# Optimization experiments

Hardware: AMD Instinct MI355X
Metric: run time of the kernel (lower is better)

## Reference

```python
import jax, jax.numpy as jnp
import numpy as np

EMBED_DIM = 1024
NUM_HEADS = 16
N = 32768


def setup_inputs() -> dict:
    key = jax.random.key(0)
    k1, k2, k3 = jax.random.split(key, 3)
    h = jax.random.normal(k1, (N, EMBED_DIM), dtype=jnp.float32)
    # torch nn.Linear(E, 3E): weight [3E, E], bias [3E] (bias=True by default)
    W_qkv = jax.random.normal(k2, (3 * EMBED_DIM, EMBED_DIM), dtype=jnp.float32) * 0.02
    b_qkv = jax.random.normal(k3, (3 * EMBED_DIM,), dtype=jnp.float32) * 0.02
    return {"h": h, "W_qkv": W_qkv, "b_qkv": b_qkv}


def reference(h, W_qkv, b_qkv):
    n, e = h.shape
    head_dim = e // NUM_HEADS
    # fused QKV projection: [N, 3E]
    qkv = h @ W_qkv.T + b_qkv
    # reshape [N, 3, H, D] -> split
    qkv = qkv.reshape(n, 3, NUM_HEADS, head_dim)
    q, k, v = qkv[:, 0], qkv[:, 1], qkv[:, 2]  # each [N, H, D]
    # NOTE: attention over the HEAD axis per token, scaled by sqrt(embed_dim)
    scores = jnp.einsum("nid,njd->nij", q, k) / (e ** 0.5)  # [N, H, H]
    attn = jax.nn.softmax(scores, axis=-1)
    out = jnp.einsum("nij,njd->nid", attn, v)  # [N, H, D]
    # faithful to torch: permute(1,0,2) then reshape(N, E) (mixes node order)
    out = jnp.transpose(out, (1, 0, 2)).reshape(n, e)
    return out
```

## Files before the change

kernel.cpp:

```cpp
#include <hip/hip_runtime.h>
#include <stdint.h>

#define NTOK 32768
#define EMB  1024
#define QKVN 3072
#define NH   16
#define HD   64

typedef __bf16 bf16x8 __attribute__((ext_vector_type(8)));
typedef float  floatx4 __attribute__((ext_vector_type(4)));
typedef unsigned int   uintx4   __attribute__((ext_vector_type(4)));
typedef unsigned short ushortx4 __attribute__((ext_vector_type(4)));
typedef unsigned short ushortx8 __attribute__((ext_vector_type(8)));

__device__ __forceinline__ unsigned short f2bf_rne(float f){
    unsigned int x; __builtin_memcpy(&x, &f, 4);
    x += 0x7fffu + ((x >> 16) & 1u);
    return (unsigned short)(x >> 16);
}

__device__ __forceinline__ void async_copy16(void* lds, const void* gsrc){
    __builtin_amdgcn_global_load_lds(
        (const __attribute__((address_space(1))) unsigned int*)gsrc,
        (__attribute__((address_space(3))) unsigned int*)lds,
        16, 0, 0);
}

__global__ __launch_bounds__(256) void cast_f32_bf16(const float* __restrict__ in,
                                                     unsigned short* __restrict__ out,
                                                     int n4){
    int idx = blockIdx.x * 256 + threadIdx.x;
    if (idx < n4){
        floatx4 v = ((const floatx4*)in)[idx];
        ushortx4 o;
        o[0] = f2bf_rne(v[0]); o[1] = f2bf_rne(v[1]);
        o[2] = f2bf_rne(v[2]); o[3] = f2bf_rne(v[3]);
        ((ushortx4*)out)[idx] = o;
    }
}


__device__ __forceinline__ void stage_a_half(unsigned short* At, const unsigned short* A,
                                             int m0, int h, int kt, int tid){
    #pragma unroll
    for (int g = 0; g < 2; g++){
        int row0  = g * 128 + h * 64;
        int rl    = tid >> 3;
        int chunk = tid & 7;
        int row   = row0 + rl;
        int k8    = chunk ^ (row & 7);
        async_copy16((char*)At + row0 * 128 + tid * 16,
                     &A[(size_t)(m0 + row) * EMB + kt + k8 * 8]);
    }
}

__device__ __forceinline__ void stage_b_half(unsigned short* Bt, const unsigned short* B,
                                             int n0, int h, int kt, int tid){
    #pragma unroll
    for (int j = 0; j < 2; j++){
        int qg    = j * 2 + (tid >> 8);
        int row0  = qg * 64 + h * 32;
        int t2    = tid & 255;
        int rl    = t2 >> 3;
        int chunk = tid & 7;
        int row   = row0 + rl;
        int k8    = chunk ^ (row & 7);
        async_copy16((char*)Bt + row0 * 128 + t2 * 16,
                     &B[(size_t)(n0 + row) * EMB + kt + k8 * 8]);
    }
}

#define LDA_HALF(H)                                                                 \
    _Pragma("unroll")                                                               \
    for (int mi = 0; mi < 4; mi++){                                                 \
        int row = wm * 128 + (H) * 64 + mi * 16 + r16;                              \
        _Pragma("unroll")                                                           \
        for (int ks = 0; ks < 2; ks++)                                              \
            a[mi][ks] = *(const bf16x8*)&curA[row * 64 + (((quad + 4*ks) ^ (row & 7)) * 8)]; \
    }

#define LDB_PAIR(NI0)                                                               \
    _Pragma("unroll")                                                               \
    for (int ni = 0; ni < 2; ni++){                                                 \
        int row = wn * 64 + ((NI0) + ni) * 16 + r16;                                \
        _Pragma("unroll")                                                           \
        for (int ks = 0; ks < 2; ks++)                                              \
            b[ni][ks] = *(const bf16x8*)&curB[row * 64 + (((quad + 4*ks) ^ (row & 7)) * 8)]; \
    }

#define MFMA16(MI0, NI0)                                                            \
    _Pragma("unroll")                                                               \
    for (int mi = 0; mi < 4; mi++)                                                  \
        _Pragma("unroll")                                                           \
        for (int ni = 0; ni < 2; ni++)                                              \
            _Pragma("unroll")                                                       \
            for (int ks = 0; ks < 2; ks++)                                          \
                acc[(MI0) + mi][(NI0) + ni] = __builtin_amdgcn_mfma_f32_16x16x32_bf16( \
                    a[mi][ks], b[ni][ks], acc[(MI0) + mi][(NI0) + ni], 0, 0, 0);

__device__ __forceinline__ void ktile_iter(const unsigned short* __restrict__ A,
                                           const unsigned short* __restrict__ B,
                                           unsigned short* curA, unsigned short* curB,
                                           unsigned short* nxtA, unsigned short* nxtB,
                                           int m0, int n0, int kt, int tid,
                                           floatx4 (&acc)[8][4]){
    const int lane = tid & 63;
    const int wave = tid >> 6;
    const int wm = wave >> 2, wn = wave & 3;
    const int r16 = lane & 15, quad = lane >> 4;
    bf16x8 a[4][2], b[2][2];

    LDA_HALF(0);
    LDB_PAIR(0);
    stage_a_half(nxtA, A, m0, 1, kt + 64, tid);
    __builtin_amdgcn_s_barrier();
    asm volatile("s_waitcnt lgkmcnt(0)" ::: "memory");
    __builtin_amdgcn_s_setprio(1);
    MFMA16(0, 0);
    __builtin_amdgcn_s_setprio(0);
    __builtin_amdgcn_s_barrier();

    LDB_PAIR(2);
    stage_b_half(nxtB, B, n0, 0, kt + 64, tid);
    __builtin_amdgcn_s_barrier();
    asm volatile("s_waitcnt lgkmcnt(0)" ::: "memory");
    __builtin_amdgcn_s_setprio(1);
    MFMA16(0, 2);
    __builtin_amdgcn_s_setprio(0);
    __builtin_amdgcn_s_barrier();

    LDA_HALF(1);
    stage_a_half(curA, A, m0, 0, kt + 128, tid);
    __builtin_amdgcn_s_barrier();
    asm volatile("s_waitcnt lgkmcnt(0)" ::: "memory");
    __builtin_amdgcn_s_setprio(1);
    MFMA16(4, 2);
    __builtin_amdgcn_s_setprio(0);
    __builtin_amdgcn_s_barrier();

    LDB_PAIR(0);
    stage_b_half(curB, B, n0, 1, kt + 128, tid);
    __builtin_amdgcn_s_barrier();
    asm volatile("s_waitcnt lgkmcnt(0)" ::: "memory");
    __builtin_amdgcn_s_setprio(1);
    MFMA16(4, 0);
    __builtin_amdgcn_s_setprio(0);
    asm volatile("s_waitcnt vmcnt(4)" ::: "memory");
    __builtin_amdgcn_s_barrier();
}

__global__ __launch_bounds__(512, 2) void qkv_gemm256(const unsigned short* __restrict__ A,
                                                      const unsigned short* __restrict__ B,
                                                      const float* __restrict__ bias,
                                                      unsigned short* __restrict__ C){
    extern __shared__ __align__(16) unsigned short lds[];
    unsigned short* A0 = lds;
    unsigned short* B0 = lds + 16384;
    unsigned short* A1 = lds + 32768;
    unsigned short* B1 = lds + 49152;

    const int tid = threadIdx.x;
    int bid = blockIdx.x;
    int swz = (bid & 7) * 192 + (bid >> 3);
    int by  = swz / 12;
    int bx  = swz - by * 12;
    const int m0 = by * 256, n0 = bx * 256;

    floatx4 acc[8][4];
    #pragma unroll
    for (int i = 0; i < 8; i++)
        #pragma unroll
        for (int j = 0; j < 4; j++) acc[i][j] = floatx4{0.f, 0.f, 0.f, 0.f};

    stage_a_half(A0, A, m0, 0, 0, tid);
    stage_a_half(A0, A, m0, 1, 0, tid);
    stage_b_half(B0, B, n0, 0, 0, tid);
    stage_b_half(B0, B, n0, 1, 0, tid);
    stage_a_half(A1, A, m0, 0, 64, tid);
    stage_b_half(B1, B, n0, 1, 64, tid);
    asm volatile("s_waitcnt vmcnt(4)" ::: "memory");
    __builtin_amdgcn_s_barrier();

    #pragma unroll 1
    for (int t = 0; t < 16; t += 2){
        ktile_iter(A, B, A0, B0, A1, B1, m0, n0, t * 64,      tid, acc);
        ktile_iter(A, B, A1, B1, A0, B0, m0, n0, t * 64 + 64, tid, acc);
    }

    const int lane = tid & 63;
    const int wave = tid >> 6;
    const int wm = wave >> 2, wn = wave & 3;
    const int r16 = lane & 15, quad = lane >> 4;
    #pragma unroll
    for (int ni = 0; ni < 4; ni++){
        int gcol = n0 + wn * 64 + ni * 16 + r16;
        float bv = bias[gcol];
        #pragma unroll
        for (int mi = 0; mi < 8; mi++){
            #pragma unroll
            for (int r = 0; r < 4; r++){
                int grow = m0 + wm * 128 + mi * 16 + quad * 4 + r;
                C[(size_t)grow * QKVN + gcol] = f2bf_rne(acc[mi][ni][r] + bv);
            }
        }
    }
}

#define TOKL 3072
#define KOFF 0
#define VOFF 1152
#define POFF 2688

__global__ __launch_bounds__(256) void attn_mfma(const unsigned short* __restrict__ qkv,
                                                 float* __restrict__ out){
    __shared__ unsigned short sm[4 * TOKL];

    const int tid = threadIdx.x;
    const int n0  = blockIdx.x * 4;

    #pragma unroll
    for (int s = 0; s < 2; s++){
        int c   = tid + s * 256;
        int t   = c >> 7;
        int rem = c & 127;
        int j   = rem >> 3;
        int d8  = (rem & 7) * 8;
        ushortx8 kk = *(const ushortx8*)&qkv[(size_t)(n0 + t) * QKVN + EMB + j * HD + d8];
        *(ushortx8*)&sm[t * TOKL + KOFF + j * 72 + d8] = kk;
        ushortx8 vv = *(const ushortx8*)&qkv[(size_t)(n0 + t) * QKVN + 2 * EMB + j * HD + d8];
        #pragma unroll
        for (int e = 0; e < 8; e++)
            sm[t * TOKL + VOFF + (d8 + e) * 24 + j] = vv[e];
    }
    __syncthreads();

    const int wave = tid >> 6;
    const int lane = tid & 63;
    const int col  = lane & 15;
    const int quad = lane >> 4;
    const int n    = n0 + wave;
    unsigned short* tb = &sm[wave * TOKL];

    const unsigned short* qrow = qkv + (size_t)n * QKVN + col * HD;
    bf16x8 qf0 = *(const bf16x8*)(qrow + quad * 8);
    bf16x8 qf1 = *(const bf16x8*)(qrow + 32 + quad * 8);
    bf16x8 kf0 = *(const bf16x8*)&tb[KOFF + col * 72 + quad * 8];
    bf16x8 kf1 = *(const bf16x8*)&tb[KOFF + col * 72 + 32 + quad * 8];

    floatx4 sAcc = floatx4{0.f, 0.f, 0.f, 0.f};
    sAcc = __builtin_amdgcn_mfma_f32_16x16x32_bf16(qf0, kf0, sAcc, 0, 0, 0);
    sAcc = __builtin_amdgcn_mfma_f32_16x16x32_bf16(qf1, kf1, sAcc, 0, 0, 0);

    #pragma unroll
    for (int r = 0; r < 4; r++){
        float sv = sAcc[r] * 0.03125f;
        float m = sv;
        m = fmaxf(m, __shfl_xor(m, 1));
        m = fmaxf(m, __shfl_xor(m, 2));
        m = fmaxf(m, __shfl_xor(m, 4));
        m = fmaxf(m, __shfl_xor(m, 8));
        float p = __expf(sv - m);
        float l = p;
        l += __shfl_xor(l, 1);
        l += __shfl_xor(l, 2);
        l += __shfl_xor(l, 4);
        l += __shfl_xor(l, 8);
        p *= 1.f / l;
        tb[POFF + (quad * 4 + r) * 24 + col] = f2bf_rne(p);
    }

    bf16x8 pf;
    #pragma unroll
    for (int z = 0; z < 8; z++) pf[z] = (__bf16)0.0f;
    if (quad < 2) pf = *(const bf16x8*)&tb[POFF + col * 24 + quad * 8];

    #pragma unroll
    for (int dblk = 0; dblk < 4; dblk++){
        bf16x8 vf;
        #pragma unroll
        for (int z = 0; z < 8; z++) vf[z] = (__bf16)0.0f;
        if (quad < 2) vf = *(const bf16x8*)&tb[VOFF + (dblk * 16 + col) * 24 + quad * 8];
        floatx4 o = __builtin_amdgcn_mfma_f32_16x16x32_bf16(
                        pf, vf, floatx4{0.f, 0.f, 0.f, 0.f}, 0, 0, 0);
        #pragma unroll
        for (int r = 0; r < 4; r++){
            int i = quad * 4 + r;
            out[(size_t)i * (NTOK * HD) + (size_t)n * HD + dblk * 16 + col] = o[r];
        }
    }
}

extern "C" void kernel_launch(void* const* d_in, const int* in_sizes, int n_in,
                              void* d_out, int out_size, void* d_ws, size_t ws_size,
                              hipStream_t stream){
    const float* h = (const float*)d_in[0];
    const float* W = (const float*)d_in[1];
    const float* b = (const float*)d_in[2];
    float* out = (float*)d_out;

    char* ws = (char*)d_ws;
    unsigned short* h_bf = (unsigned short*)ws;
    unsigned short* w_bf = (unsigned short*)(ws + (size_t)64 * 1024 * 1024);
    unsigned short* qkv  = (unsigned short*)(ws + (size_t)72 * 1024 * 1024);

    static bool attr_set = false;
    if (!attr_set){
        hipFuncSetAttribute(reinterpret_cast<const void*>(qkv_gemm256),
                            hipFuncAttributeMaxDynamicSharedMemorySize, 131072);
        attr_set = true;
    }

    cast_f32_bf16<<<(NTOK * EMB / 4 + 255) / 256, 256, 0, stream>>>(h, h_bf, NTOK * EMB / 4);
    cast_f32_bf16<<<(QKVN * EMB / 4 + 255) / 256, 256, 0, stream>>>(W, w_bf, QKVN * EMB / 4);

    qkv_gemm256<<<dim3(1536), 512, 131072, stream>>>(h_bf, w_bf, b, qkv);

    attn_mfma<<<NTOK / 4, 256, 0, stream>>>(qkv, out);
}
```

Baseline: 521.9 us.

## Restructure QKV GEMM k-loop into 8-phase pipeline with register-carried fragments

The GEMM main loop is reorganised from four 16-MFMA phases into eight 8-MFMA phases. A fragments are loaded in quarter-tiles into ping-pong registers (aX/aY), and B fragments are kept in registers across phases and preloaded from the next buffer. Global-to-LDS staging is split into smaller quarter chunks, and the first k-tile's fragments are loaded before the loop, so LDS reads, async copies and MFMA overlap more finely. In exchange there are more barriers per k-tile, higher register pressure from the carried fragments, and more intricate vmcnt accounting that could break correctness if the counts are wrong.

```diff
diff --git a/kernel.cpp b/kernel.cpp
--- a/kernel.cpp
+++ b/kernel.cpp
@@ -40,18 +40,15 @@
 }
 
 
-__device__ __forceinline__ void stage_a_half(unsigned short* At, const unsigned short* A,
-                                             int m0, int h, int kt, int tid){
-    #pragma unroll
-    for (int g = 0; g < 2; g++){
-        int row0  = g * 128 + h * 64;
-        int rl    = tid >> 3;
-        int chunk = tid & 7;
-        int row   = row0 + rl;
-        int k8    = chunk ^ (row & 7);
-        async_copy16((char*)At + row0 * 128 + tid * 16,
-                     &A[(size_t)(m0 + row) * EMB + kt + k8 * 8]);
-    }
+__device__ __forceinline__ void stage_a_q(unsigned short* At, const unsigned short* A,
+                                          int m0, int q, int kt, int tid){
+    int g     = tid >> 8;
+    int rl    = (tid & 255) >> 3;
+    int chunk = tid & 7;
+    int row   = g * 128 + q * 32 + rl;
+    int k8    = chunk ^ (row & 7);
+    async_copy16((char*)At + row * 128 + chunk * 16,
+                 &A[(size_t)(m0 + row) * EMB + kt + k8 * 8]);
 }
 
 __device__ __forceinline__ void stage_b_half(unsigned short* Bt, const unsigned short* B,
@@ -70,83 +67,82 @@
     }
 }
 
-#define LDA_HALF(H)                                                                 \
+#define LDA_Q(DST, BUF, Q)                                                          \
     _Pragma("unroll")                                                               \
-    for (int mi = 0; mi < 4; mi++){                                                 \
-        int row = wm * 128 + (H) * 64 + mi * 16 + r16;                              \
+    for (int mi = 0; mi < 2; mi++){                                                 \
+        int row = wm * 128 + (Q) * 32 + mi * 16 + r16;                              \
         _Pragma("unroll")                                                           \
         for (int ks = 0; ks < 2; ks++)                                              \
-            a[mi][ks] = *(const bf16x8*)&curA[row * 64 + (((quad + 4*ks) ^ (row & 7)) * 8)]; \
-    }
-
-#define LDB_PAIR(NI0)                                                               \
+            DST[mi][ks] = *(const bf16x8*)&(BUF)[row * 64 + (((quad + 4*ks) ^ (row & 7)) * 8)]; \
+    }
+
+#define LDB_P(DST, BUF, P)                                                          \
     _Pragma("unroll")                                                               \
     for (int ni = 0; ni < 2; ni++){                                                 \
-        int row = wn * 64 + ((NI0) + ni) * 16 + r16;                                \
+        int row = wn * 64 + (P) * 32 + ni * 16 + r16;                               \
         _Pragma("unroll")                                                           \
         for (int ks = 0; ks < 2; ks++)                                              \
-            b[ni][ks] = *(const bf16x8*)&curB[row * 64 + (((quad + 4*ks) ^ (row & 7)) * 8)]; \
-    }
-
-#define MFMA16(MI0, NI0)                                                            \
+            DST[ni][ks] = *(const bf16x8*)&(BUF)[row * 64 + (((quad + 4*ks) ^ (row & 7)) * 8)]; \
+    }
+
+#define MFMA8(Q, P, AS, BS)                                                         \
     _Pragma("unroll")                                                               \
-    for (int mi = 0; mi < 4; mi++)                                                  \
+    for (int mi = 0; mi < 2; mi++)                                                  \
         _Pragma("unroll")                                                           \
         for (int ni = 0; ni < 2; ni++)                                              \
             _Pragma("unroll")                                                       \
             for (int ks = 0; ks < 2; ks++)                                          \
-                acc[(MI0) + mi][(NI0) + ni] = __builtin_amdgcn_mfma_f32_16x16x32_bf16( \
-                    a[mi][ks], b[ni][ks], acc[(MI0) + mi][(NI0) + ni], 0, 0, 0);
-
-__device__ __forceinline__ void ktile_iter(const unsigned short* __restrict__ A,
-                                           const unsigned short* __restrict__ B,
-                                           unsigned short* curA, unsigned short* curB,
-                                           unsigned short* nxtA, unsigned short* nxtB,
-                                           int m0, int n0, int kt, int tid,
-                                           floatx4 (&acc)[8][4]){
+                acc[(Q)*2 + mi][(P)*2 + ni] = __builtin_amdgcn_mfma_f32_16x16x32_bf16( \
+                    AS[mi][ks], BS[ni][ks], acc[(Q)*2 + mi][(P)*2 + ni], 0, 0, 0);
+
+#define SETP1 __builtin_amdgcn_s_setprio(1)
+#define SETP0 __builtin_amdgcn_s_setprio(0)
+#define BAR   __builtin_amdgcn_s_barrier()
+
+__device__ __forceinline__ void ktile8(const unsigned short* __restrict__ A,
+                                       const unsigned short* __restrict__ B,
+                                       unsigned short* curA, unsigned short* curB,
+                                       unsigned short* nxtA, unsigned short* nxtB,
+                                       int m0, int n0, int kt, int tid,
+                                       bf16x8 (&aX)[2][2], bf16x8 (&aY)[2][2],
+                                       bf16x8 (&b01)[2][2], bf16x8 (&b23)[2][2],
+                                       floatx4 (&acc)[8][4]){
     const int lane = tid & 63;
     const int wave = tid >> 6;
     const int wm = wave >> 2, wn = wave & 3;
     const int r16 = lane & 15, quad = lane >> 4;
-    bf16x8 a[4][2], b[2][2];
-
-    LDA_HALF(0);
-    LDB_PAIR(0);
-    stage_a_half(nxtA, A, m0, 1, kt + 64, tid);
-    __builtin_amdgcn_s_barrier();
-    asm volatile("s_waitcnt lgkmcnt(0)" ::: "memory");
-    __builtin_amdgcn_s_setprio(1);
-    MFMA16(0, 0);
-    __builtin_amdgcn_s_setprio(0);
-    __builtin_amdgcn_s_barrier();
-
-    LDB_PAIR(2);
-    stage_b_half(nxtB, B, n0, 0, kt + 64, tid);
-    __builtin_amdgcn_s_barrier();
-    asm volatile("s_waitcnt lgkmcnt(0)" ::: "memory");
-    __builtin_amdgcn_s_setprio(1);
-    MFMA16(0, 2);
-    __builtin_amdgcn_s_setprio(0);
-    __builtin_amdgcn_s_barrier();
-
-    LDA_HALF(1);
-    stage_a_half(curA, A, m0, 0, kt + 128, tid);
-    __builtin_amdgcn_s_barrier();
-    asm volatile("s_waitcnt lgkmcnt(0)" ::: "memory");
-    __builtin_amdgcn_s_setprio(1);
-    MFMA16(4, 2);
-    __builtin_amdgcn_s_setprio(0);
-    __builtin_amdgcn_s_barrier();
-
-    LDB_PAIR(0);
-    stage_b_half(curB, B, n0, 1, kt + 128, tid);
-    __builtin_amdgcn_s_barrier();
-    asm volatile("s_waitcnt lgkmcnt(0)" ::: "memory");
-    __builtin_amdgcn_s_setprio(1);
-    MFMA16(4, 0);
-    __builtin_amdgcn_s_setprio(0);
-    asm volatile("s_waitcnt vmcnt(4)" ::: "memory");
-    __builtin_amdgcn_s_barrier();
+    const int ks2 = kt + 128;
+
+    SETP1; MFMA8(0, 0, aX, b01); SETP0; BAR;
+
+    LDA_Q(aY, curA, 1);
+    stage_a_q(curA, A, m0, 0, ks2, tid);
+    stage_b_half(curB, B, n0, 0, ks2, tid);
+    SETP1; MFMA8(0, 1, aX, b23); SETP0; BAR;
+
+    stage_b_half(curB, B, n0, 1, ks2, tid);
+    SETP1; MFMA8(1, 1, aY, b23); SETP0; BAR;
+
+    LDA_Q(aX, curA, 2);
+    stage_a_q(curA, A, m0, 1, ks2, tid);
+    SETP1; MFMA8(1, 0, aY, b01); SETP0; BAR;
+
+    SETP1; MFMA8(2, 0, aX, b01); SETP0; BAR;
+
+    LDA_Q(aY, curA, 3);
+    stage_a_q(curA, A, m0, 2, ks2, tid);
+    SETP1; MFMA8(2, 1, aX, b23); SETP0; BAR;
+
+    SETP1; MFMA8(3, 1, aY, b23); SETP0;
+    asm volatile("s_waitcnt vmcnt(7)" ::: "memory");
+    BAR;
+
+    LDB_P(b23, nxtB, 1);
+    LDA_Q(aX, nxtA, 0);
+    SETP1; MFMA8(3, 0, aY, b01); SETP0;
+    LDB_P(b01, nxtB, 0);
+    stage_a_q(curA, A, m0, 3, ks2, tid);
+    BAR;
 }
 
 __global__ __launch_bounds__(512, 2) void qkv_gemm256(const unsigned short* __restrict__ A,
@@ -166,31 +162,39 @@
     int bx  = swz - by * 12;
     const int m0 = by * 256, n0 = bx * 256;
 
-    floatx4 acc[8][4];
-    #pragma unroll
-    for (int i = 0; i < 8; i++)
-        #pragma unroll
-        for (int j = 0; j < 4; j++) acc[i][j] = floatx4{0.f, 0.f, 0.f, 0.f};
-
-    stage_a_half(A0, A, m0, 0, 0, tid);
-    stage_a_half(A0, A, m0, 1, 0, tid);
-    stage_b_half(B0, B, n0, 0, 0, tid);
-    stage_b_half(B0, B, n0, 1, 0, tid);
-    stage_a_half(A1, A, m0, 0, 64, tid);
-    stage_b_half(B1, B, n0, 1, 64, tid);
-    asm volatile("s_waitcnt vmcnt(4)" ::: "memory");
-    __builtin_amdgcn_s_barrier();
-
-    #pragma unroll 1
-    for (int t = 0; t < 16; t += 2){
-        ktile_iter(A, B, A0, B0, A1, B1, m0, n0, t * 64,      tid, acc);
-        ktile_iter(A, B, A1, B1, A0, B0, m0, n0, t * 64 + 64, tid, acc);
-    }
-
     const int lane = tid & 63;
     const int wave = tid >> 6;
     const int wm = wave >> 2, wn = wave & 3;
     const int r16 = lane & 15, quad = lane >> 4;
+
+    floatx4 acc[8][4];
+    #pragma unroll
+    for (int i = 0; i < 8; i++)
+        #pragma unroll
+        for (int j = 0; j < 4; j++) acc[i][j] = floatx4{0.f, 0.f, 0.f, 0.f};
+
+    #pragma unroll
+    for (int q = 0; q < 4; q++) stage_a_q(A0, A, m0, q, 0, tid);
+    stage_b_half(B0, B, n0, 0, 0, tid);
+    stage_b_half(B0, B, n0, 1, 0, tid);
+    #pragma unroll
+    for (int q = 0; q < 4; q++) stage_a_q(A1, A, m0, q, 64, tid);
+    stage_b_half(B1, B, n0, 0, 64, tid);
+    stage_b_half(B1, B, n0, 1, 64, tid);
+    asm volatile("s_waitcnt vmcnt(8)" ::: "memory");
+    BAR;
+
+    bf16x8 aX[2][2], aY[2][2], b01[2][2], b23[2][2];
+    LDA_Q(aX, A0, 0);
+    LDB_P(b01, B0, 0);
+    LDB_P(b23, B0, 1);
+
+    #pragma unroll 1
+    for (int t = 0; t < 16; t += 2){
+        ktile8(A, B, A0, B0, A1, B1, m0, n0, t * 64,      tid, aX, aY, b01, b23, acc);
+        ktile8(A, B, A1, B1, A0, B0, m0, n0, t * 64 + 64, tid, aX, aY, b01, b23, acc);
+    }
+
     #pragma unroll
     for (int ni = 0; ni < 4; ni++){
         int gcol = n0 + wn * 64 + ni * 16 + r16;
```

After: 511.5 us. -2.0%, faster.
